# Optimization experiments

Measured on AMD Instinct MI355X. Metric: run time of the kernel, lower is better.

## Reference

```python
import jax, jax.numpy as jnp
import numpy as np


def log_g(x):
    # log of g(x) = where(x>=0, x+0.5, sigmoid(x))
    return jnp.where(x >= 0, jnp.log(jax.nn.relu(x) + 0.5), -jax.nn.softplus(-x))


def heinsen_scan_log(log_coeffs, log_values):
    # associative scan in log space over seq dim (axis=1)
    a_star = jnp.cumsum(log_coeffs, axis=1)
    log_h0_plus_b_star = jax.lax.cumlogsumexp(log_values - a_star, axis=1)
    return jnp.exp(a_star + log_h0_plus_b_star)


def setup_inputs() -> dict:
    key = jax.random.key(0)
    k1, k2, k3 = jax.random.split(key, 3)
    B, S, D_IN, D_INNER, D_OUT = 4, 4096, 1024, 1024, 1024
    x = jax.random.normal(k1, (B, S, D_IN), dtype=jnp.float32)
    # xavier_normal for Linear(d_in, 2*d_inner): std = sqrt(2/(fan_in+fan_out))
    std_hg = float(np.sqrt(2.0 / (D_IN + 2 * D_INNER)))
    W_hg = jax.random.normal(k2, (2 * D_INNER, D_IN), dtype=jnp.float32) * std_hg
    std_out = float(np.sqrt(2.0 / (D_INNER + D_OUT)))
    W_out = jax.random.normal(k3, (D_OUT, D_INNER), dtype=jnp.float32) * std_out
    return {"x": x, "W_hg": W_hg, "W_out": W_out}


def reference(x, W_hg, W_out):
    # x: [B,S,Din]; W_hg: [2*Dinner, Din]; W_out: [Dout, Dinner]
    hg = jnp.einsum("bsd,ed->bse", x, W_hg)
    hidden, gate = jnp.split(hg, 2, axis=-1)
    log_coeffs = -jax.nn.softplus(gate)        # log(1 - z)
    log_z = -jax.nn.softplus(-gate)            # log(z)
    log_values = log_z + log_g(hidden)
    h = heinsen_scan_log(log_coeffs, log_values)  # [B,S,Dinner]
    out = jnp.einsum("bsd,od->bso", h, W_out)
    return out
```

## Files before the change

kernel.cpp:

```cpp
#include <hip/hip_runtime.h>
#include <math.h>


typedef unsigned short ushort_t;
typedef unsigned int uint_t;
typedef __attribute__((ext_vector_type(4))) float f32x4;
typedef __attribute__((ext_vector_type(8))) __bf16 bf16x8;
typedef __attribute__((ext_vector_type(8))) unsigned short u16x8;

constexpr int Bsz  = 4;
constexpr int S    = 4096;
constexpr int Din  = 1024;
constexpr int Dh   = 1024;
constexpr int M    = Bsz * S;
constexpr int NCH  = 64;
constexpr int CL   = S / NCH;

__device__ __forceinline__ unsigned short f2bf(float f) {
    unsigned int u = __float_as_uint(f);
    unsigned int r = (u + 0x7fffu + ((u >> 16) & 1u)) >> 16;
    return (unsigned short)r;
}
__device__ __forceinline__ float bf2f(unsigned short u) {
    return __uint_as_float(((unsigned int)u) << 16);
}
__device__ __forceinline__ float sigf(float x) {
    x = fminf(fmaxf(x, -30.f), 30.f);
    return 1.0f / (1.0f + __expf(-x));
}
__device__ __forceinline__ void gld_lds16(const ushort_t* g, ushort_t* l) {
    __builtin_amdgcn_global_load_lds(
        (const __attribute__((address_space(1))) void*)g,
        (__attribute__((address_space(3))) void*)l, 16, 0, 0);
}

__global__ __launch_bounds__(256) void cvt_all(
    const float* __restrict__ x, const float* __restrict__ whg,
    const float* __restrict__ wout,
    ushort_t* __restrict__ xb, ushort_t* __restrict__ whgb,
    ushort_t* __restrict__ woutb)
{
    constexpr int NX = M * Din / 8;
    constexpr int NW = 2048 * 1024 / 8;
    const int i = blockIdx.x * 256 + threadIdx.x;
    const float* src; ushort_t* dst; int k;
    if (i < NX)            { src = x;    dst = xb;    k = i; }
    else if (i < NX + NW)  { src = whg;  dst = whgb;  k = i - NX; }
    else                   { src = wout; dst = woutb; k = i - NX - NW; }
    const float4 a = ((const float4*)src)[(size_t)k * 2];
    const float4 b = ((const float4*)src)[(size_t)k * 2 + 1];
    u16x8 o;
    o[0] = f2bf(a.x); o[1] = f2bf(a.y); o[2] = f2bf(a.z); o[3] = f2bf(a.w);
    o[4] = f2bf(b.x); o[5] = f2bf(b.y); o[6] = f2bf(b.z); o[7] = f2bf(b.w);
    ((u16x8*)dst)[k] = o;
}

__global__ __launch_bounds__(512, 2) void gemm256(
    const ushort_t* __restrict__ A, int lda,
    const ushort_t* __restrict__ B, int ldb,
    ushort_t* __restrict__ Cout, int ldc, int K, int nbx_log2)
{
    __shared__ ushort_t lds[4][2][8192];

    const int P = K >> 5;

    const int nwg = gridDim.x;
    const int cpx = nwg >> 3;
    const int bid = blockIdx.x;
    const int swz = (bid & 7) * cpx + (bid >> 3);
    const int bx  = swz & ((1 << nbx_log2) - 1);
    const int by  = swz >> nbx_log2;
    const int bm0 = by * 256;
    const int bn0 = bx * 256;

    const int t  = threadIdx.x;
    const int w  = t >> 6;
    const int l  = t & 63;
    const int wr = w >> 2;
    const int wc = w & 3;

    const int fr = l & 15;
    const int kg = l >> 4;
    const int qp = kg ^ (((fr >> 3) & 1) << 1);
    const int a_base = wr * 4096 + fr * 32 + qp * 8;
    const int b_base = wc * 2048 + fr * 32 + qp * 8;

    const int rs = l >> 2;
    const int lq = (l & 3) ^ (((rs >> 3) & 1) << 1);
    const ushort_t* gA0 = A + (size_t)(bm0 + w * 16 + rs) * lda + lq * 8;
    const ushort_t* gA1 = gA0 + (size_t)128 * lda;
    const ushort_t* gB0 = B + (size_t)(bn0 + w * 16 + rs) * ldb + lq * 8;
    const ushort_t* gB1 = gB0 + (size_t)128 * ldb;

    f32x4 acc[8][4];
    #pragma unroll
    for (int i = 0; i < 8; ++i)
        #pragma unroll
        for (int j = 0; j < 4; ++j)
            acc[i][j] = (f32x4){0.f, 0.f, 0.f, 0.f};

    auto stage = [&](int p) {
        const int s2 = p & 3;
        const int ko = p * 32;
        gld_lds16(gA0 + ko, &lds[s2][0][w * 512]);
        gld_lds16(gA1 + ko, &lds[s2][0][w * 512 + 4096]);
        gld_lds16(gB0 + ko, &lds[s2][1][w * 512]);
        gld_lds16(gB1 + ko, &lds[s2][1][w * 512 + 4096]);
    };

    auto phase_body = [&](int p, bool do_stage) {
        __builtin_amdgcn_s_barrier();
        __builtin_amdgcn_sched_barrier(0);
        const int s = p & 3;
        const ushort_t* la = &lds[s][0][0];
        const ushort_t* lb = &lds[s][1][0];
        bf16x8 af[8], bfr[4];
        #pragma unroll
        for (int i = 0; i < 8; ++i)
            af[i] = *reinterpret_cast<const bf16x8*>(&la[a_base + i * 512]);
        #pragma unroll
        for (int j = 0; j < 4; ++j)
            bfr[j] = *reinterpret_cast<const bf16x8*>(&lb[b_base + j * 512]);
        if (do_stage) stage(p + 2);
        __builtin_amdgcn_sched_barrier(0);
        __builtin_amdgcn_s_setprio(1);
        #pragma unroll
        for (int i = 0; i < 8; ++i)
            #pragma unroll
            for (int j = 0; j < 4; ++j)
                acc[i][j] = __builtin_amdgcn_mfma_f32_16x16x32_bf16(
                    af[i], bfr[j], acc[i][j], 0, 0, 0);
        __builtin_amdgcn_s_setprio(0);
        __builtin_amdgcn_sched_barrier(0);
    };

    stage(0);
    stage(1);

    for (int p = 0; p < P - 1; ++p) {
        asm volatile("s_waitcnt vmcnt(4)" ::: "memory");
        phase_body(p, p < P - 2);
    }
    asm volatile("s_waitcnt vmcnt(0)" ::: "memory");
    phase_body(P - 1, false);

    #pragma unroll
    for (int i = 0; i < 8; ++i) {
        #pragma unroll
        for (int j = 0; j < 4; ++j) {
            const int col = bn0 + wc * 64 + j * 16 + fr;
            #pragma unroll
            for (int r = 0; r < 4; ++r) {
                const int row = bm0 + wr * 128 + i * 16 + kg * 4 + r;
                Cout[(size_t)row * ldc + col] = f2bf(acc[i][j][r]);
            }
        }
    }
}

__global__ __launch_bounds__(256) void gemm2w4(
    const ushort_t* __restrict__ A, int lda,
    const ushort_t* __restrict__ B, int ldb,
    float* __restrict__ Cout, int ldc, int K, int nbx_log2)
{
    __shared__ ushort_t lds[3][12288];

    const int P = K >> 5;

    const int nwg = gridDim.x;
    const int cpx = nwg >> 3;
    const int bid = blockIdx.x;
    const int swz = (bid & 7) * cpx + (bid >> 3);
    const int bx  = swz & ((1 << nbx_log2) - 1);
    const int by  = swz >> nbx_log2;
    const int bm0 = by * 128;
    const int bn0 = bx * 256;

    const int t = threadIdx.x;
    const int w = t >> 6;
    const int l = t & 63;

    const int fr = l & 15;
    const int kg = l >> 4;
    const int qp = kg ^ (((fr >> 3) & 1) << 1);
    const int a_base = fr * 32 + qp * 8;
    const int b_base = 4096 + w * 2048 + fr * 32 + qp * 8;

    const int rs = l >> 2;
    const int lq = (l & 3) ^ (((rs >> 3) & 1) << 1);
    const ushort_t* gA0 = A + (size_t)(bm0 + w * 32 + rs) * lda + lq * 8;
    const ushort_t* gA1 = gA0 + (size_t)16 * lda;
    const ushort_t* gB0 = B + (size_t)(bn0 + w * 64 + rs) * ldb + lq * 8;
    const ushort_t* gB1 = gB0 + (size_t)16 * ldb;
    const ushort_t* gB2 = gB0 + (size_t)32 * ldb;
    const ushort_t* gB3 = gB0 + (size_t)48 * ldb;

    f32x4 acc[8][4];
    #pragma unroll
    for (int i = 0; i < 8; ++i)
        #pragma unroll
        for (int j = 0; j < 4; ++j)
            acc[i][j] = (f32x4){0.f, 0.f, 0.f, 0.f};

    auto stage = [&](int p, int s) {
        ushort_t* base = &lds[s][0];
        const int ko = p * 32;
        gld_lds16(gA0 + ko, base + w * 1024);
        gld_lds16(gA1 + ko, base + w * 1024 + 512);
        gld_lds16(gB0 + ko, base + 4096 + w * 2048);
        gld_lds16(gB1 + ko, base + 4096 + w * 2048 + 512);
        gld_lds16(gB2 + ko, base + 4096 + w * 2048 + 1024);
        gld_lds16(gB3 + ko, base + 4096 + w * 2048 + 1536);
    };

    auto phase_body = [&](int p, int s, int s2, bool do_stage) {
        __builtin_amdgcn_s_barrier();
        __builtin_amdgcn_sched_barrier(0);
        const ushort_t* ls = &lds[s][0];
        bf16x8 af[8], bfr[4];
        #pragma unroll
        for (int i = 0; i < 8; ++i)
            af[i] = *reinterpret_cast<const bf16x8*>(&ls[a_base + i * 512]);
        #pragma unroll
        for (int j = 0; j < 4; ++j)
            bfr[j] = *reinterpret_cast<const bf16x8*>(&ls[b_base + j * 512]);
        if (do_stage) stage(p + 2, s2);
        __builtin_amdgcn_sched_barrier(0);
        __builtin_amdgcn_s_setprio(1);
        #pragma unroll
        for (int i = 0; i < 8; ++i)
            #pragma unroll
            for (int j = 0; j < 4; ++j)
                acc[i][j] = __builtin_amdgcn_mfma_f32_16x16x32_bf16(
                    af[i], bfr[j], acc[i][j], 0, 0, 0);
        __builtin_amdgcn_s_setprio(0);
        __builtin_amdgcn_sched_barrier(0);
    };

    stage(0, 0);
    stage(1, 1);

    int scur = 0, snx2 = 2;
    #pragma unroll 1
    for (int p = 0; p < P - 1; ++p) {
        asm volatile("s_waitcnt vmcnt(6)" ::: "memory");
        phase_body(p, scur, snx2, p < P - 2);
        scur = (scur == 2) ? 0 : scur + 1;
        snx2 = (snx2 == 2) ? 0 : snx2 + 1;
    }
    asm volatile("s_waitcnt vmcnt(0)" ::: "memory");
    phase_body(P - 1, scur, snx2, false);

    #pragma unroll
    for (int i = 0; i < 8; ++i) {
        #pragma unroll
        for (int j = 0; j < 4; ++j) {
            const int col = bn0 + w * 64 + j * 16 + fr;
            #pragma unroll
            for (int r = 0; r < 4; ++r) {
                const int row = bm0 + i * 16 + kg * 4 + r;
                Cout[(size_t)row * ldc + col] = acc[i][j][r];
            }
        }
    }
}


__global__ __launch_bounds__(256) void scan_stage1(
    const ushort_t* __restrict__ hg, float* __restrict__ Abuf,
    float* __restrict__ hlbuf)
{
    const int bid   = blockIdx.x;
    const int half  = bid & 1;
    const int chunk = (bid >> 1) & (NCH - 1);
    const int b     = bid >> 7;
    const int t     = threadIdx.x;
    const int d     = half * 512 + 2 * t;
    const size_t rowbase = (size_t)(b * S + chunk * CL) * 2048 + d;

    float h0 = 0.f, h1 = 0.f, A0 = 1.f, A1 = 1.f;
    #pragma unroll 4
    for (int i = 0; i < CL; ++i) {
        const ushort_t* rp = hg + rowbase + (size_t)i * 2048;
        const uint_t hp = *(const uint_t*)rp;
        const uint_t gp = *(const uint_t*)(rp + 1024);
        const float hid0 = bf2f((ushort_t)hp), hid1 = bf2f((ushort_t)(hp >> 16));
        const float g0 = bf2f((ushort_t)gp),  g1 = bf2f((ushort_t)(gp >> 16));
        const float c0 = sigf(-g0), z0 = 1.f - c0;
        const float c1 = sigf(-g1), z1 = 1.f - c1;
        const float gv0 = (hid0 >= 0.f) ? (hid0 + 0.5f) : sigf(hid0);
        const float gv1 = (hid1 >= 0.f) ? (hid1 + 0.5f) : sigf(hid1);
        h0 = fmaf(c0, h0, z0 * gv0);  A0 *= c0;
        h1 = fmaf(c1, h1, z1 * gv1);  A1 *= c1;
    }
    const size_t pb = (size_t)(b * NCH + chunk) * 1024 + d;
    *(float2*)&Abuf[pb]  = make_float2(A0, A1);
    *(float2*)&hlbuf[pb] = make_float2(h0, h1);
}

__global__ __launch_bounds__(256) void scan_stage2(
    const float* __restrict__ Abuf, const float* __restrict__ hlbuf,
    float* __restrict__ Hs)
{
    const int g = blockIdx.x * 256 + threadIdx.x;
    const int d = g & (Dh - 1);
    const int b = g >> 10;
    float h = 0.0f;
    for (int ch = 0; ch < NCH; ++ch) {
        const size_t o = (size_t)(b * NCH + ch) * Dh + d;
        Hs[o] = h;
        h = fmaf(Abuf[o], h, hlbuf[o]);
    }
}

__global__ __launch_bounds__(256) void scan_stage3(
    const ushort_t* __restrict__ hg, const float* __restrict__ Hs,
    ushort_t* __restrict__ hout)
{
    const int bid   = blockIdx.x;
    const int half  = bid & 1;
    const int chunk = (bid >> 1) & (NCH - 1);
    const int b     = bid >> 7;
    const int t     = threadIdx.x;
    const int d     = half * 512 + 2 * t;
    const size_t rowbase = (size_t)(b * S + chunk * CL) * 2048 + d;
    const size_t hb      = (size_t)(b * S + chunk * CL) * 1024 + d;

    const float2 hs = *(const float2*)&Hs[(size_t)(b * NCH + chunk) * 1024 + d];
    float h0 = hs.x, h1 = hs.y;
    #pragma unroll 4
    for (int i = 0; i < CL; ++i) {
        const ushort_t* rp = hg + rowbase + (size_t)i * 2048;
        const uint_t hp = *(const uint_t*)rp;
        const uint_t gp = *(const uint_t*)(rp + 1024);
        const float hid0 = bf2f((ushort_t)hp), hid1 = bf2f((ushort_t)(hp >> 16));
        const float g0 = bf2f((ushort_t)gp),  g1 = bf2f((ushort_t)(gp >> 16));
        const float c0 = sigf(-g0), z0 = 1.f - c0;
        const float c1 = sigf(-g1), z1 = 1.f - c1;
        const float gv0 = (hid0 >= 0.f) ? (hid0 + 0.5f) : sigf(hid0);
        const float gv1 = (hid1 >= 0.f) ? (hid1 + 0.5f) : sigf(hid1);
        h0 = fmaf(c0, h0, z0 * gv0);
        h1 = fmaf(c1, h1, z1 * gv1);
        const uint_t o = (uint_t)f2bf(h0) | ((uint_t)f2bf(h1) << 16);
        *(uint_t*)(hout + hb + (size_t)i * 1024) = o;
    }
}

extern "C" void kernel_launch(void* const* d_in, const int* in_sizes, int n_in,
                              void* d_out, int out_size, void* d_ws, size_t ws_size,
                              hipStream_t stream)
{
    (void)in_sizes; (void)n_in; (void)out_size; (void)ws_size;
    const float* x    = (const float*)d_in[0];
    const float* Whg  = (const float*)d_in[1];
    const float* Wout = (const float*)d_in[2];
    float* out = (float*)d_out;

    ushort_t* hgbuf = (ushort_t*)d_ws;
    ushort_t* xb    = hgbuf + (size_t)M * 2048;
    ushort_t* whgb  = xb + (size_t)M * 1024;
    ushort_t* woutb = whgb + (size_t)2048 * 1024;
    float*    Abuf  = (float*)(woutb + (size_t)1024 * 1024);
    float*    hlbuf = Abuf + (size_t)Bsz * NCH * Dh;
    float*    Hsbuf = hlbuf + (size_t)Bsz * NCH * Dh;

    const dim3 blk(256);

    cvt_all<<<dim3(9728), blk, 0, stream>>>(x, Whg, Wout, xb, whgb, woutb);

    gemm256<<<dim3(512), dim3(512), 0, stream>>>(
        xb, Din, whgb, Din, hgbuf, 2048, Din, 3);

    scan_stage1<<<dim3(512), blk, 0, stream>>>(hgbuf, Abuf, hlbuf);
    scan_stage2<<<dim3(Bsz * Dh / 256), blk, 0, stream>>>(Abuf, hlbuf, Hsbuf);
    scan_stage3<<<dim3(512), blk, 0, stream>>>(hgbuf, Hsbuf, xb);

    gemm2w4<<<dim3(512), blk, 0, stream>>>(
        xb, Dh, woutb, Din, out, 1024, Dh, 2);
}
```

Measured before the change: 207.7 us.

## Fuse three scan stages into one kernel with grid-wide atomic barriers

```diff
diff --git a/kernel.cpp b/kernel.cpp
--- a/kernel.cpp
+++ b/kernel.cpp
@@ -265,10 +265,10 @@
     }
 }
 
-
-__global__ __launch_bounds__(256) void scan_stage1(
+__global__ __launch_bounds__(256) void scan_fused3(
     const ushort_t* __restrict__ hg, float* __restrict__ Abuf,
-    float* __restrict__ hlbuf)
+    float* __restrict__ hlbuf, float* __restrict__ Hs,
+    int* __restrict__ cnt, ushort_t* __restrict__ hout)
 {
     const int bid   = blockIdx.x;
     const int half  = bid & 1;
@@ -296,38 +296,46 @@
     const size_t pb = (size_t)(b * NCH + chunk) * 1024 + d;
     *(float2*)&Abuf[pb]  = make_float2(A0, A1);
     *(float2*)&hlbuf[pb] = make_float2(h0, h1);
-}
-
-__global__ __launch_bounds__(256) void scan_stage2(
-    const float* __restrict__ Abuf, const float* __restrict__ hlbuf,
-    float* __restrict__ Hs)
-{
-    const int g = blockIdx.x * 256 + threadIdx.x;
-    const int d = g & (Dh - 1);
-    const int b = g >> 10;
-    float h = 0.0f;
-    for (int ch = 0; ch < NCH; ++ch) {
-        const size_t o = (size_t)(b * NCH + ch) * Dh + d;
-        Hs[o] = h;
-        h = fmaf(Abuf[o], h, hlbuf[o]);
-    }
-}
-
-__global__ __launch_bounds__(256) void scan_stage3(
-    const ushort_t* __restrict__ hg, const float* __restrict__ Hs,
-    ushort_t* __restrict__ hout)
-{
-    const int bid   = blockIdx.x;
-    const int half  = bid & 1;
-    const int chunk = (bid >> 1) & (NCH - 1);
-    const int b     = bid >> 7;
-    const int t     = threadIdx.x;
-    const int d     = half * 512 + 2 * t;
-    const size_t rowbase = (size_t)(b * S + chunk * CL) * 2048 + d;
-    const size_t hb      = (size_t)(b * S + chunk * CL) * 1024 + d;
-
+
+    __syncthreads();
+    if (t == 0) {
+        __threadfence();
+        __hip_atomic_fetch_add(&cnt[0], 1, __ATOMIC_ACQ_REL,
+                               __HIP_MEMORY_SCOPE_AGENT);
+        while (__hip_atomic_load(&cnt[0], __ATOMIC_ACQUIRE,
+                                 __HIP_MEMORY_SCOPE_AGENT) < 512)
+            __builtin_amdgcn_s_sleep(2);
+        __threadfence();
+    }
+    __syncthreads();
+
+    if (bid < 16) {
+        const int g  = bid * 256 + t;
+        const int d2 = g & (Dh - 1);
+        const int b2 = g >> 10;
+        float h = 0.0f;
+        for (int ch = 0; ch < NCH; ++ch) {
+            const size_t o = (size_t)(b2 * NCH + ch) * Dh + d2;
+            Hs[o] = h;
+            h = fmaf(Abuf[o], h, hlbuf[o]);
+        }
+    }
+
+    __syncthreads();
+    if (t == 0) {
+        __threadfence();
+        __hip_atomic_fetch_add(&cnt[1], 1, __ATOMIC_ACQ_REL,
+                               __HIP_MEMORY_SCOPE_AGENT);
+        while (__hip_atomic_load(&cnt[1], __ATOMIC_ACQUIRE,
+                                 __HIP_MEMORY_SCOPE_AGENT) < 512)
+            __builtin_amdgcn_s_sleep(2);
+        __threadfence();
+    }
+    __syncthreads();
+
+    const size_t hb = (size_t)(b * S + chunk * CL) * 1024 + d;
     const float2 hs = *(const float2*)&Hs[(size_t)(b * NCH + chunk) * 1024 + d];
-    float h0 = hs.x, h1 = hs.y;
+    h0 = hs.x; h1 = hs.y;
     #pragma unroll 4
     for (int i = 0; i < CL; ++i) {
         const ushort_t* rp = hg + rowbase + (size_t)i * 2048;
@@ -363,17 +371,19 @@
     float*    Abuf  = (float*)(woutb + (size_t)1024 * 1024);
     float*    hlbuf = Abuf + (size_t)Bsz * NCH * Dh;
     float*    Hsbuf = hlbuf + (size_t)Bsz * NCH * Dh;
+    int*      cnt   = (int*)(Hsbuf + (size_t)Bsz * NCH * Dh);
 
     const dim3 blk(256);
+
+    hipMemsetAsync(cnt, 0, 2 * sizeof(int), stream);
 
     cvt_all<<<dim3(9728), blk, 0, stream>>>(x, Whg, Wout, xb, whgb, woutb);
 
     gemm256<<<dim3(512), dim3(512), 0, stream>>>(
         xb, Din, whgb, Din, hgbuf, 2048, Din, 3);
 
-    scan_stage1<<<dim3(512), blk, 0, stream>>>(hgbuf, Abuf, hlbuf);
-    scan_stage2<<<dim3(Bsz * Dh / 256), blk, 0, stream>>>(Abuf, hlbuf, Hsbuf);
-    scan_stage3<<<dim3(512), blk, 0, stream>>>(hgbuf, Hsbuf, xb);
+    scan_fused3<<<dim3(512), blk, 0, stream>>>(
+        hgbuf, Abuf, hlbuf, Hsbuf, cnt, xb);
 
     gemm2w4<<<dim3(512), blk, 0, stream>>>(
         xb, Dh, woutb, Din, out, 1024, Dh, 2);
```

Result: slower. 360.7 us (+73.7%).
